# Kernel tuning notes

Hardware: AMD Instinct MI355X
Metric: run time of the kernel (lower is better)

## Reference

```python
import jax, jax.numpy as jnp
import numpy as np

H = 16      # headNum
C = 64      # cDim
D = 1024    # qDim = kDim = vDim = outDim
N = 2       # batch
S = 1024    # seq len


def setup_inputs() -> dict:
    key = jax.random.key(0)
    ks = jax.random.split(key, 12)
    inp = {
        "Qin": jax.random.normal(ks[0], (N, S, D), dtype=jnp.float32),
        "Kin": jax.random.normal(ks[1], (N, S, D), dtype=jnp.float32),
        "Vin": jax.random.normal(ks[2], (N, S, D), dtype=jnp.float32),
        "seqMask": jax.random.randint(ks[3], (N, S), 0, 2).astype(jnp.bool_),
        "attMask": jax.random.normal(ks[4], (1, 1, S, S), dtype=jnp.float32),
        # learned parameters (stored as [in, out] for x @ W)
        "QTrans": jax.random.normal(ks[5], (D, H * C), dtype=jnp.float32) * 0.02,
        "KTrans": jax.random.normal(ks[6], (D, H * C), dtype=jnp.float32) * 0.02,
        "VTrans": jax.random.normal(ks[7], (D, H * C), dtype=jnp.float32) * 0.02,
        "GTrans_w": jax.random.normal(ks[8], (D, H * C), dtype=jnp.float32) * 0.02,
        "GTrans_b": jnp.ones((H * C,), dtype=jnp.float32),
        "out_w": jax.random.normal(ks[9], (H * C, D), dtype=jnp.float32) * 0.02,
        "out_b": jnp.zeros((D,), dtype=jnp.float32),
    }
    return inp


def _split_heads(x):
    # [n, s, h*c] -> [h, n, s, c]
    n, s, _ = x.shape
    return x.reshape(n, s, H, C).transpose(2, 0, 1, 3)


def reference(Qin, Kin, Vin, seqMask, attMask, QTrans, KTrans, VTrans,
              GTrans_w, GTrans_b, out_w, out_b):
    Q = _split_heads(Qin @ QTrans)                         # [h,n,s,c]
    K = _split_heads(Kin @ KTrans)                         # [h,n,t,c]
    V = _split_heads(Vin @ VTrans)                         # [h,n,t,c]
    G = jax.nn.sigmoid(_split_heads(Vin @ GTrans_w + GTrans_b))  # [h,n,s,c]

    scale = 1.0 / jnp.sqrt(jnp.float32(C))
    A = jnp.einsum('hnsi,hnti->hnst', Q, K) * scale        # [h,n,s,t]
    # masked_fill where outer-product of seqMask is True
    m = (seqMask[:, :, None] & seqMask[:, None, :])[None]  # [1,n,s,t]
    A = jnp.where(m, -jnp.inf, A)
    A = A + attMask
    A = jax.nn.softmax(A, axis=-1)
    # gated attention-value reduction (eval mode: dropout inactive)
    O = jnp.einsum('hnst,hnti,hnsi->nshi', A, V, G)        # [n,s,h,c]
    O = O.reshape(O.shape[0], O.shape[1], -1)              # [n,s,h*c]
    return O @ out_w + out_b
```

## Files before the change

kernel.cpp:

```cpp
#include <hip/hip_runtime.h>
#include <hip/hip_bf16.h>
#include <cstddef>

#define S_   1024
#define HC_  1024
#define C_   64
#define LOG2E 1.4426950408889634f
#define SC2   0.18033688011112042f

typedef __attribute__((ext_vector_type(8))) short bf16x8;
typedef __attribute__((ext_vector_type(4))) short bf16x4;
typedef __attribute__((ext_vector_type(4))) float f32x4;

typedef __attribute__((address_space(1))) const void gconst_t;
typedef __attribute__((address_space(3))) void lds_t;

__device__ __forceinline__ short cvt_bf16(float f) {
  union { float f; unsigned u; } v; v.f = f;
  unsigned r = v.u + 0x7FFFu + ((v.u >> 16) & 1u);
  return (short)(r >> 16);
}
__device__ __forceinline__ float bf2f(short s) {
  union { float f; unsigned u; } v; v.u = ((unsigned)(unsigned short)s) << 16;
  return v.f;
}

template<int N> __device__ __forceinline__ void wait_vm() {
  if constexpr (N == 0)       asm volatile("s_waitcnt vmcnt(0)" ::: "memory");
  else if constexpr (N == 2)  asm volatile("s_waitcnt vmcnt(2)" ::: "memory");
  else if constexpr (N == 4)  asm volatile("s_waitcnt vmcnt(4)" ::: "memory");
  else if constexpr (N == 6)  asm volatile("s_waitcnt vmcnt(6)" ::: "memory");
  else if constexpr (N == 8)  asm volatile("s_waitcnt vmcnt(8)" ::: "memory");
  else if constexpr (N == 12) asm volatile("s_waitcnt vmcnt(12)" ::: "memory");
}

__global__ __launch_bounds__(256) void prep(
    const float* __restrict__ QT, const float* __restrict__ KT,
    const float* __restrict__ VT, const float* __restrict__ GW,
    const float* __restrict__ OW, short* __restrict__ WTb,
    const float* __restrict__ Qin, const float* __restrict__ Kin,
    const float* __restrict__ Vin, short* __restrict__ Abf,
    const float* __restrict__ att, const unsigned char* __restrict__ sm,
    short* __restrict__ biasP) {
  __shared__ short tile[32][33];
  __shared__ int a1, a4;
  const int bid = blockIdx.x;
  const int t = threadIdx.x;

  if (bid < 5120) {
    const int which = bid >> 10, xb = bid & 1023;
    const float* src = (which == 0) ? QT : (which == 1) ? KT : (which == 2) ? VT
                      : (which == 3) ? GW : OW;
    short* dst = WTb + (size_t)which * (1024u * 1024u);
    const int tj = (xb & 31) * 32;
    const int tk = (xb >> 5) * 32;
    const int r = t >> 3, c4 = (t & 7) * 4;
    const float4 v = *(const float4*)(src + (size_t)(tk + r) * 1024 + tj + c4);
    tile[c4 + 0][r] = cvt_bf16(v.x);
    tile[c4 + 1][r] = cvt_bf16(v.y);
    tile[c4 + 2][r] = cvt_bf16(v.z);
    tile[c4 + 3][r] = cvt_bf16(v.w);
    __syncthreads();
    bf16x4 o;
    o[0] = tile[r][c4 + 0]; o[1] = tile[r][c4 + 1];
    o[2] = tile[r][c4 + 2]; o[3] = tile[r][c4 + 3];
    *(bf16x4*)(dst + (size_t)(tj + r) * 1024 + tk + c4) = o;
  } else if (bid < 8192) {
    const int idx = bid - 5120;
    const int y = idx >> 10, xb = idx & 1023;
    const float* src = (y == 0) ? Qin : (y == 1) ? Kin : Vin;
    short* d = Abf + (size_t)y * 2097152u;
    const int i = (xb * 256 + t) * 8;
    const float4 a = *(const float4*)(src + i);
    const float4 b = *(const float4*)(src + i + 4);
    bf16x8 o;
    o[0] = cvt_bf16(a.x); o[1] = cvt_bf16(a.y); o[2] = cvt_bf16(a.z); o[3] = cvt_bf16(a.w);
    o[4] = cvt_bf16(b.x); o[5] = cvt_bf16(b.y); o[6] = cvt_bf16(b.z); o[7] = cvt_bf16(b.w);
    *(bf16x8*)(d + i) = o;
  } else {
    if (t == 0) { a1 = 0; a4 = 0; }
    __syncthreads();
    int l1 = 0, l4 = 0;
    for (int i = t; i < 2048; i += 256) {
      if (sm[i]) { if (i & 3) l1 = 1; else if (i & 4) l4 = 1; }
    }
    if (l1) atomicOr(&a1, 1);
    if (l4) atomicOr(&a4, 1);
    __syncthreads();
    const int mst = a1 ? 1 : (a4 ? 4 : 8);

    const int idx = bid - 8192;
    const int qw = idx & 63, tt = (idx >> 6) & 15, n = idx >> 10;
    const int lslot = t >> 2, i4 = t & 3;
    const int tc = tt * 64 + i4 * 16 + (lslot & 15);
    const int qbase = qw * 16 + ((lslot >> 4) << 2);
    const int smt = sm[(size_t)(n * 1024 + tc) * mst];
    bf16x4 o;
#pragma unroll
    for (int ii = 0; ii < 4; ii++) {
      const int q = qbase + ii;
      const int smq = sm[(size_t)(n * 1024 + q) * mst];
      const float val = (smq && smt) ? -1e4f : att[(size_t)q * 1024 + tc] * LOG2E;
      o[ii] = cvt_bf16(val);
    }
    short* dst = biasP + (((size_t)(n * 64 + qw) * 16 + tt) * 64 + lslot) * 16 + i4 * 4;
    *(bf16x4*)dst = o;
  }
}

__global__ __launch_bounds__(256) void v_transpose(
    const short* __restrict__ Vp, short* __restrict__ VpT) {
  __shared__ short tile[32][33];
  const int n = blockIdx.y;
  const int tc = (blockIdx.x & 31) * 32;
  const int ts = (blockIdx.x >> 5) * 32;
  const int t = threadIdx.x;
  const int r = t >> 3, c4 = (t & 7) * 4;
  bf16x4 v = *(const bf16x4*)(Vp + (size_t)(n * S_ + ts + r) * HC_ + tc + c4);
  tile[c4 + 0][r] = v[0]; tile[c4 + 1][r] = v[1];
  tile[c4 + 2][r] = v[2]; tile[c4 + 3][r] = v[3];
  __syncthreads();
  bf16x4 o;
  o[0] = tile[r][c4 + 0]; o[1] = tile[r][c4 + 1];
  o[2] = tile[r][c4 + 2]; o[3] = tile[r][c4 + 3];
  *(bf16x4*)(VpT + ((size_t)n * HC_ + tc + r) * S_ + ts + c4) = o;
}

template<int MW, int NW>
__device__ __forceinline__ void gemm_core_bf(
    const short* __restrict__ A, const short* __restrict__ BT,
    short* As, short* Bs, int m0, int n0, f32x4 acc[MW][NW]) {
  const int t = threadIdx.x;
  const int lane = t & 63, wid = t >> 6;
  const int wr = wid >> 1, wc = wid & 1;
  const int l15 = lane & 15, g = lane >> 4;
  constexpr int NT = 32;
  constexpr int LDT = MW / 2 + NW / 2;
  constexpr int ABUF = MW * 1024;
  constexpr int BBUF = NW * 1024;

#pragma unroll
  for (int m = 0; m < MW; m++)
#pragma unroll
    for (int n2 = 0; n2 < NW; n2++) acc[m][n2] = (f32x4){0.f, 0.f, 0.f, 0.f};

#define STAGE_(buf, kt)                                                        \
  {                                                                            \
    const int k0_ = (kt) * 32;                                                 \
    _Pragma("unroll")                                                          \
    for (int i_ = 0; i_ < NW / 2; i_++) {                                      \
      const int seg_ = i_ * 256 + t;                                           \
      const int row_ = seg_ >> 2, gl_ = seg_ & 3;                              \
      __builtin_amdgcn_global_load_lds(                                        \
          (gconst_t*)(BT + (size_t)(n0 + row_) * 1024 + k0_ +                  \
                      ((gl_ ^ ((row_ >> 1) & 3)) * 8)),                        \
          (lds_t*)(Bs + (buf) * BBUF + seg_ * 8), 16, 0, 0);                   \
    }                                                                          \
    _Pragma("unroll")                                                          \
    for (int i_ = 0; i_ < MW / 2; i_++) {                                      \
      const int seg_ = i_ * 256 + t;                                           \
      const int row_ = seg_ >> 2, gl_ = seg_ & 3;                              \
      __builtin_amdgcn_global_load_lds(                                        \
          (gconst_t*)(A + (size_t)(m0 + row_) * 1024 + k0_ +                   \
                      ((gl_ ^ ((row_ >> 1) & 3)) * 8)),                        \
          (lds_t*)(As + (buf) * ABUF + seg_ * 8), 16, 0, 0);                   \
    }                                                                          \
  }

  STAGE_(0, 0);
  STAGE_(1, 1);
  STAGE_(2, 2);
  int b0 = 0, b1 = 1, b2 = 2, b3 = 3;
  for (int kt = 0; kt < NT; ++kt) {
    if (kt + 3 < NT) {
      STAGE_(b3, kt + 3);
      wait_vm<3 * LDT>();
    } else if (kt + 3 == NT) {
      wait_vm<2 * LDT>();
    } else if (kt + 2 == NT) {
      wait_vm<LDT>();
    } else {
      wait_vm<0>();
    }
    __builtin_amdgcn_sched_barrier(0);
    __builtin_amdgcn_s_barrier();
    __builtin_amdgcn_sched_barrier(0);

    const short* Ac = As + b0 * ABUF;
    const short* Bc = Bs + b0 * BBUF;
    bf16x8 a[MW], b[NW];
#pragma unroll
    for (int m = 0; m < MW; m++) {
      const int row = wr * (MW * 16) + m * 16 + l15;
      a[m] = *(const bf16x8*)(Ac + row * 32 + ((g ^ ((row >> 1) & 3)) * 8));
    }
#pragma unroll
    for (int n2 = 0; n2 < NW; n2++) {
      const int row = wc * (NW * 16) + n2 * 16 + l15;
      b[n2] = *(const bf16x8*)(Bc + row * 32 + ((g ^ ((row >> 1) & 3)) * 8));
    }
    __builtin_amdgcn_s_setprio(1);
#pragma unroll
    for (int m = 0; m < MW; m++)
#pragma unroll
      for (int n2 = 0; n2 < NW; n2++)
        acc[m][n2] = __builtin_amdgcn_mfma_f32_16x16x32_bf16(a[m], b[n2], acc[m][n2], 0, 0, 0);
    __builtin_amdgcn_s_setprio(0);
    __builtin_amdgcn_sched_barrier(0);
    __builtin_amdgcn_s_barrier();
    __builtin_amdgcn_sched_barrier(0);
    const int tmp = b0; b0 = b1; b1 = b2; b2 = b3; b3 = tmp;
  }
#undef STAGE_
}

__global__ __launch_bounds__(256) void gemm_proj(
    const short* __restrict__ Abf, const short* __restrict__ WTb,
    short* __restrict__ Pb, const float* __restrict__ gb) {
  __shared__ short As[4 * 4096];
  __shared__ short Bs[4 * 4096];
  const int bid = blockIdx.x;
  const int xcd = bid & 7, ord = bid >> 3;
  const int y = xcd >> 1, nh = xcd & 1;
  const int m0 = (ord & 15) * 128;
  const int n0 = (nh * 4 + (ord >> 4)) * 128;
  const short* A = Abf + (size_t)((y <= 2) ? y : 2) * 2097152u;
  const short* BT = WTb + (size_t)y * (1024u * 1024u);
  short* outp = Pb + (size_t)y * 2097152u;
  f32x4 acc[4][4];
  gemm_core_bf<4, 4>(A, BT, As, Bs, m0, n0, acc);
  const int t = threadIdx.x, lane = t & 63, wid = t >> 6;
  const int wr = wid >> 1, wc = wid & 1, l15 = lane & 15, g = lane >> 4;
#pragma unroll
  for (int m = 0; m < 4; m++)
#pragma unroll
    for (int n2 = 0; n2 < 4; n2++)
#pragma unroll
      for (int j = 0; j < 4; j++) {
        const int row = m0 + wr * 64 + m * 16 + g * 4 + j;
        const int col = n0 + wc * 64 + n2 * 16 + l15;
        float v = acc[m][n2][j];
        if (y == 3) { v += gb[col]; v = 1.0f / (1.0f + __expf(-v)); }
        outp[(size_t)row * 1024 + col] = cvt_bf16(v);
      }
}

__global__ __launch_bounds__(256) void gemm_final(
    const short* __restrict__ Aobuf, const short* __restrict__ WTo,
    float* __restrict__ outp, const float* __restrict__ ob) {
  __shared__ short As[4 * 2048];
  __shared__ short Bs[4 * 2048];
  const int bid = blockIdx.x;
  const int xcd = bid & 7, ord = bid >> 3;
  const int mg = xcd >> 1, ng = xcd & 1;
  const int m0 = (mg * 8 + (ord & 7)) * 64;
  const int n0 = (ng * 8 + (ord >> 3)) * 64;
  f32x4 acc[2][2];
  gemm_core_bf<2, 2>(Aobuf, WTo, As, Bs, m0, n0, acc);
  const int t = threadIdx.x, lane = t & 63, wid = t >> 6;
  const int wr = wid >> 1, wc = wid & 1, l15 = lane & 15, g = lane >> 4;
#pragma unroll
  for (int m = 0; m < 2; m++)
#pragma unroll
    for (int n2 = 0; n2 < 2; n2++)
#pragma unroll
      for (int j = 0; j < 4; j++) {
        const int row = m0 + wr * 32 + m * 16 + g * 4 + j;
        const int col = n0 + wc * 32 + n2 * 16 + l15;
        outp[(size_t)row * 1024 + col] = acc[m][n2][j] + ob[col];
      }
}

__global__ __launch_bounds__(256) void attn_split(
    const short* __restrict__ Qp, const short* __restrict__ Kp,
    const short* __restrict__ VpT, const short* __restrict__ biasP,
    float* __restrict__ mlbuf, short* __restrict__ OpartB, int lns) {
  __shared__ short Ks[64 * 64];
  __shared__ short Vt[64 * 64];
  __shared__ short Pl[4][16 * 64];

  const int t = threadIdx.x;
  const int lane = t & 63, w = t >> 6;
  const int l15 = lane & 15, g = lane >> 4;
  const int xb = blockIdx.x, h = blockIdx.y, n = blockIdx.z;
  const int sp = xb & ((1 << lns) - 1), qb = xb >> lns;
  const int itc = 16 >> lns;

  const int sbase = qb * 64 + w * 16;
  const short* qptr = Qp + (size_t)(n * S_ + sbase + l15) * HC_ + h * C_;
  const bf16x8 qf0 = *(const bf16x8*)(qptr + g * 8);
  const bf16x8 qf1 = *(const bf16x8*)(qptr + 32 + g * 8);

  float mrow[4], lsum[4];
  f32x4 oacc[4];
#pragma unroll
  for (int j = 0; j < 4; j++) { mrow[j] = -1e30f; lsum[j] = 0.f; }
#pragma unroll
  for (int cb = 0; cb < 4; cb++) oacc[cb] = (f32x4){0.f, 0.f, 0.f, 0.f};

  const int str = t >> 3, sc8 = (t & 7) * 8;
  const short* bbase = biasP + ((size_t)(n * 64 + qb * 4 + w) * 16 * 64 + lane) * 16;

  {
    const int t0 = sp * itc * 64;
    bf16x8 kA0 = *(const bf16x8*)(Kp + (size_t)(n * S_ + t0 + str) * HC_ + h * C_ + sc8);
    bf16x8 kA1 = *(const bf16x8*)(Kp + (size_t)(n * S_ + t0 + 32 + str) * HC_ + h * C_ + sc8);
    bf16x8 vA0 = *(const bf16x8*)(VpT + ((size_t)n * HC_ + h * C_ + str) * S_ + t0 + sc8);
    bf16x8 vA1 = *(const bf16x8*)(VpT + ((size_t)n * HC_ + h * C_ + 32 + str) * S_ + t0 + sc8);

    for (int it = 0; it < itc; ++it) {
      const int tg = sp * itc + it;
      __syncthreads();
      { const int kr = str;      *(bf16x8*)((char*)Ks + kr * 128 + ((sc8 * 2) ^ ((kr & 7) << 4))) = kA0; }
      { const int kr = 32 + str; *(bf16x8*)((char*)Ks + kr * 128 + ((sc8 * 2) ^ ((kr & 7) << 4))) = kA1; }
      { const int cr = str;      *(bf16x8*)((char*)Vt + cr * 128 + ((sc8 * 2) ^ ((cr & 7) << 4))) = vA0; }
      { const int cr = 32 + str; *(bf16x8*)((char*)Vt + cr * 128 + ((sc8 * 2) ^ ((cr & 7) << 4))) = vA1; }
      __syncthreads();

      const bf16x8 bf0 = *(const bf16x8*)(bbase + tg * 1024);
      const bf16x8 bf1 = *(const bf16x8*)(bbase + tg * 1024 + 8);
      const int t1 = ((it + 1 < itc) ? (tg + 1) : tg) * 64;
      bf16x8 kB0 = *(const bf16x8*)(Kp + (size_t)(n * S_ + t1 + str) * HC_ + h * C_ + sc8);
      bf16x8 kB1 = *(const bf16x8*)(Kp + (size_t)(n * S_ + t1 + 32 + str) * HC_ + h * C_ + sc8);
      bf16x8 vB0 = *(const bf16x8*)(VpT + ((size_t)n * HC_ + h * C_ + str) * S_ + t1 + sc8);
      bf16x8 vB1 = *(const bf16x8*)(VpT + ((size_t)n * HC_ + h * C_ + 32 + str) * S_ + t1 + sc8);

      f32x4 sacc[4];
#pragma unroll
      for (int nb = 0; nb < 4; nb++) sacc[nb] = (f32x4){0.f, 0.f, 0.f, 0.f};
      __builtin_amdgcn_s_setprio(1);
#pragma unroll
      for (int nb = 0; nb < 4; nb++) {
        const int krow = nb * 16 + l15;
        const bf16x8 b0 = *(const bf16x8*)((char*)Ks + krow * 128 + ((g * 16) ^ ((krow & 7) << 4)));
        const bf16x8 b1 = *(const bf16x8*)((char*)Ks + krow * 128 + ((64 + g * 16) ^ ((krow & 7) << 4)));
        sacc[nb] = __builtin_amdgcn_mfma_f32_16x16x32_bf16(qf0, b0, sacc[nb], 0, 0, 0);
        sacc[nb] = __builtin_amdgcn_mfma_f32_16x16x32_bf16(qf1, b1, sacc[nb], 0, 0, 0);
      }
      __builtin_amdgcn_s_setprio(0);

      float tmax[4];
#pragma unroll
      for (int j = 0; j < 4; j++) tmax[j] = -1e30f;
#pragma unroll
      for (int nb = 0; nb < 4; nb++)
#pragma unroll
        for (int j = 0; j < 4; j++) {
          const short bb = (nb < 2) ? bf0[nb * 4 + j] : bf1[(nb - 2) * 4 + j];
          const float lg = sacc[nb][j] * SC2 + bf2f(bb);
          sacc[nb][j] = lg;
          tmax[j] = fmaxf(tmax[j], lg);
        }
#pragma unroll
      for (int j = 0; j < 4; j++) {
#pragma unroll
        for (int d = 1; d < 16; d <<= 1)
          tmax[j] = fmaxf(tmax[j], __shfl_xor(tmax[j], d, 64));
        const float mn = fmaxf(mrow[j], tmax[j]);
        const float sc = exp2f(mrow[j] - mn);
        mrow[j] = mn;
        lsum[j] *= sc;
#pragma unroll
        for (int cb = 0; cb < 4; cb++) oacc[cb][j] *= sc;
        float ps = 0.f;
#pragma unroll
        for (int nb = 0; nb < 4; nb++) {
          const float p = exp2f(sacc[nb][j] - mn);
          sacc[nb][j] = p;
          ps += p;
        }
        lsum[j] += ps;
      }
      short* Pw = &Pl[w][0];
#pragma unroll
      for (int nb = 0; nb < 4; nb++)
#pragma unroll
        for (int j = 0; j < 4; j++) {
          const int pr = g * 4 + j;
          const int pcb = (nb * 16 + l15) * 2;
          *(short*)((char*)Pw + pr * 128 + (pcb ^ ((pr & 7) << 4))) = cvt_bf16(sacc[nb][j]);
        }
      __builtin_amdgcn_s_setprio(1);
#pragma unroll
      for (int kk = 0; kk < 2; kk++) {
        const bf16x8 pf = *(const bf16x8*)((char*)Pw + l15 * 128 + ((kk * 64 + g * 16) ^ ((l15 & 7) << 4)));
#pragma unroll
        for (int cb = 0; cb < 4; cb++) {
          const int vrow = cb * 16 + l15;
          const bf16x8 vf = *(const bf16x8*)((char*)Vt + vrow * 128 + ((kk * 64 + g * 16) ^ ((vrow & 7) << 4)));
          oacc[cb] = __builtin_amdgcn_mfma_f32_16x16x32_bf16(pf, vf, oacc[cb], 0, 0, 0);
        }
      }
      __builtin_amdgcn_s_setprio(0);
      kA0 = kB0; kA1 = kB1; vA0 = vB0; vA1 = vB1;
    }
  }
  const int slot = (((n * 16 + h) * 16 + qb) << lns) + sp;
  short* op = OpartB + (size_t)slot * 4096;
  float* mlp = mlbuf + (size_t)slot * 128;
#pragma unroll
  for (int j = 0; j < 4; j++) {
    float rs = lsum[j];
#pragma unroll
    for (int d = 1; d < 16; d <<= 1) rs += __shfl_xor(rs, d, 64);
    const int row = w * 16 + g * 4 + j;
#pragma unroll
    for (int cb = 0; cb < 4; cb++)
      op[row * 64 + cb * 16 + l15] = cvt_bf16(oacc[cb][j]);
    if (l15 == 0) { mlp[row * 2] = mrow[j]; mlp[row * 2 + 1] = rs; }
  }
}

__global__ __launch_bounds__(256) void attn_merge(
    const short* __restrict__ OpartB, const float* __restrict__ mlbuf,
    const short* __restrict__ Gp, short* __restrict__ ObufB, int lns) {
  const int qb = blockIdx.x, h = blockIdx.y, n = blockIdx.z;
  const int nsplit = 1 << lns;
  const int t = threadIdx.x;
  const int r = t >> 2, c0 = (t & 3) * 16;
  const int bslot = ((n * 16 + h) * 16 + qb) << lns;
  const float* mlb = mlbuf + (size_t)bslot * 128 + r * 2;

  float M = -1e30f;
  for (int sp = 0; sp < nsplit; sp++) M = fmaxf(M, mlb[(size_t)sp * 128]);
  float l = 0.f;
  for (int sp = 0; sp < nsplit; sp++)
    l += exp2f(mlb[(size_t)sp * 128] - M) * mlb[(size_t)sp * 128 + 1];
  const float inv = 1.0f / l;

  float acc[16];
#pragma unroll
  for (int k = 0; k < 16; k++) acc[k] = 0.f;
  for (int sp = 0; sp < nsplit; sp++) {
    const float wsc = exp2f(mlb[(size_t)sp * 128] - M);
    const short* op = OpartB + (size_t)(bslot + sp) * 4096 + r * 64 + c0;
    const bf16x8 v0 = *(const bf16x8*)(op);
    const bf16x8 v1 = *(const bf16x8*)(op + 8);
#pragma unroll
    for (int k = 0; k < 8; k++) {
      acc[k]     += wsc * bf2f(v0[k]);
      acc[8 + k] += wsc * bf2f(v1[k]);
    }
  }
  const int srow = qb * 64 + r;
  const size_t idx = (size_t)(n * S_ + srow) * HC_ + h * C_ + c0;
  const bf16x8 g0 = *(const bf16x8*)(Gp + idx);
  const bf16x8 g1 = *(const bf16x8*)(Gp + idx + 8);
  bf16x8 o0, o1;
#pragma unroll
  for (int k = 0; k < 8; k++) {
    o0[k] = cvt_bf16(acc[k] * inv * bf2f(g0[k]));
    o1[k] = cvt_bf16(acc[8 + k] * inv * bf2f(g1[k]));
  }
  *(bf16x8*)(ObufB + idx) = o0;
  *(bf16x8*)(ObufB + idx + 8) = o1;
}

extern "C" void kernel_launch(void* const* d_in, const int* in_sizes, int n_in,
                              void* d_out, int out_size, void* d_ws, size_t ws_size,
                              hipStream_t stream) {
  const float* Qin      = (const float*)d_in[0];
  const float* Kin      = (const float*)d_in[1];
  const float* Vin      = (const float*)d_in[2];
  const void*  seqMask  = d_in[3];
  const float* attMask  = (const float*)d_in[4];
  const float* QTrans   = (const float*)d_in[5];
  const float* KTrans   = (const float*)d_in[6];
  const float* VTrans   = (const float*)d_in[7];
  const float* GTrans_w = (const float*)d_in[8];
  const float* GTrans_b = (const float*)d_in[9];
  const float* out_w    = (const float*)d_in[10];
  const float* out_b    = (const float*)d_in[11];
  float* out = (float*)d_out;

  char* ws = (char*)d_ws;
  const size_t MB = 1048576u;
  short* WTb   = (short*)(ws);
  short* Abf   = (short*)(ws + 10 * MB);
  short* Pb    = (short*)(ws + 22 * MB);
  short* VpT   = (short*)(ws + 38 * MB);
  short* ObufB = (short*)(ws + 42 * MB);
  short* biasP = (short*)(ws + 46 * MB);
  const size_t partBase = 51 * MB;

  const short* Kp = Pb + (size_t)1u * 2097152u;
  const short* Gp = Pb + (size_t)3u * 2097152u;

  int lns = 0;
  for (int c = 2; c >= 0; c--) {
    const size_t slots = 512u << c;
    if (ws_size >= partBase + slots * (8192u + 512u)) { lns = c; break; }
  }
  const size_t slots = 512u << lns;
  short* OpartB = (short*)(ws + partBase);
  float* mlbuf  = (float*)(ws + partBase + slots * 8192u);

  hipLaunchKernelGGL(prep, dim3(10240), dim3(256), 0, stream,
                     QTrans, KTrans, VTrans, GTrans_w, out_w, WTb,
                     Qin, Kin, Vin, Abf,
                     attMask, (const unsigned char*)seqMask, biasP);
  hipLaunchKernelGGL(gemm_proj, dim3(512), dim3(256), 0, stream,
                     Abf, WTb, Pb, GTrans_b);
  hipLaunchKernelGGL(v_transpose, dim3(1024, 2), dim3(256), 0, stream,
                     Pb + (size_t)2u * 2097152u, VpT);
  hipLaunchKernelGGL(attn_split, dim3(16 << lns, 16, 2), dim3(256), 0, stream,
                     Pb, Kp, VpT, biasP, mlbuf, OpartB, lns);
  hipLaunchKernelGGL(attn_merge, dim3(16, 16, 2), dim3(256), 0, stream,
                     OpartB, mlbuf, Gp, ObufB, lns);
  hipLaunchKernelGGL(gemm_final, dim3(512), dim3(256), 0, stream,
                     ObufB, WTb + (size_t)4u * 1048576u, out, out_b);
}
```

Before: 118.2 us.

## Fuse V transpose into projection GEMM epilogue and cap attention split count

The V-projection blocks of gemm_proj now transpose their output tile through LDS and write V directly in the transposed [n, hc, s] layout, so the separate v_transpose kernel and its extra read/write pass over V are removed. The maximum key-split factor for attention drops from 4 to 2, which lowers the partial-output traffic and merge work at the cost of fewer parallel blocks. The transposed store uses 16-byte vector writes from a 128x128 LDS tile that reuses the A staging buffer. That staging write is strided and may cause LDS bank conflicts.

```diff
diff --git a/kernel.cpp b/kernel.cpp
--- a/kernel.cpp
+++ b/kernel.cpp
@@ -108,24 +108,6 @@
   }
 }
 
-__global__ __launch_bounds__(256) void v_transpose(
-    const short* __restrict__ Vp, short* __restrict__ VpT) {
-  __shared__ short tile[32][33];
-  const int n = blockIdx.y;
-  const int tc = (blockIdx.x & 31) * 32;
-  const int ts = (blockIdx.x >> 5) * 32;
-  const int t = threadIdx.x;
-  const int r = t >> 3, c4 = (t & 7) * 4;
-  bf16x4 v = *(const bf16x4*)(Vp + (size_t)(n * S_ + ts + r) * HC_ + tc + c4);
-  tile[c4 + 0][r] = v[0]; tile[c4 + 1][r] = v[1];
-  tile[c4 + 2][r] = v[2]; tile[c4 + 3][r] = v[3];
-  __syncthreads();
-  bf16x4 o;
-  o[0] = tile[r][c4 + 0]; o[1] = tile[r][c4 + 1];
-  o[2] = tile[r][c4 + 2]; o[3] = tile[r][c4 + 3];
-  *(bf16x4*)(VpT + ((size_t)n * HC_ + tc + r) * S_ + ts + c4) = o;
-}
-
 template<int MW, int NW>
 __device__ __forceinline__ void gemm_core_bf(
     const short* __restrict__ A, const short* __restrict__ BT,
@@ -216,7 +198,8 @@
 
 __global__ __launch_bounds__(256) void gemm_proj(
     const short* __restrict__ Abf, const short* __restrict__ WTb,
-    short* __restrict__ Pb, const float* __restrict__ gb) {
+    short* __restrict__ Pb, short* __restrict__ VpT,
+    const float* __restrict__ gb) {
   __shared__ short As[4 * 4096];
   __shared__ short Bs[4 * 4096];
   const int bid = blockIdx.x;
@@ -226,23 +209,48 @@
   const int n0 = (nh * 4 + (ord >> 4)) * 128;
   const short* A = Abf + (size_t)((y <= 2) ? y : 2) * 2097152u;
   const short* BT = WTb + (size_t)y * (1024u * 1024u);
-  short* outp = Pb + (size_t)y * 2097152u;
   f32x4 acc[4][4];
   gemm_core_bf<4, 4>(A, BT, As, Bs, m0, n0, acc);
   const int t = threadIdx.x, lane = t & 63, wid = t >> 6;
   const int wr = wid >> 1, wc = wid & 1, l15 = lane & 15, g = lane >> 4;
-#pragma unroll
-  for (int m = 0; m < 4; m++)
-#pragma unroll
-    for (int n2 = 0; n2 < 4; n2++)
-#pragma unroll
-      for (int j = 0; j < 4; j++) {
-        const int row = m0 + wr * 64 + m * 16 + g * 4 + j;
-        const int col = n0 + wc * 64 + n2 * 16 + l15;
-        float v = acc[m][n2][j];
-        if (y == 3) { v += gb[col]; v = 1.0f / (1.0f + __expf(-v)); }
-        outp[(size_t)row * 1024 + col] = cvt_bf16(v);
-      }
+
+  if (y == 2) {
+    short* Tr = As;
+#pragma unroll
+    for (int m = 0; m < 4; m++)
+#pragma unroll
+      for (int n2 = 0; n2 < 4; n2++)
+#pragma unroll
+        for (int j = 0; j < 4; j++) {
+          const int r = wr * 64 + m * 16 + g * 4 + j;
+          const int c = wc * 64 + n2 * 16 + l15;
+          Tr[c * 128 + r] = cvt_bf16(acc[m][n2][j]);
+        }
+    __syncthreads();
+    const int nz = (m0 >= 1024) ? 1 : 0;
+    const int sbase = m0 & 1023;
+#pragma unroll
+    for (int p = 0; p < 8; p++) {
+      const int unit = p * 256 + t;
+      const int cl = unit >> 4, sr8 = unit & 15;
+      const bf16x8 v = *(const bf16x8*)(Tr + cl * 128 + sr8 * 8);
+      *(bf16x8*)(VpT + ((size_t)(nz * 1024 + n0 + cl)) * 1024 + sbase + sr8 * 8) = v;
+    }
+  } else {
+    short* outp = Pb + (size_t)y * 2097152u;
+#pragma unroll
+    for (int m = 0; m < 4; m++)
+#pragma unroll
+      for (int n2 = 0; n2 < 4; n2++)
+#pragma unroll
+        for (int j = 0; j < 4; j++) {
+          const int row = m0 + wr * 64 + m * 16 + g * 4 + j;
+          const int col = n0 + wc * 64 + n2 * 16 + l15;
+          float v = acc[m][n2][j];
+          if (y == 3) { v += gb[col]; v = 1.0f / (1.0f + __expf(-v)); }
+          outp[(size_t)row * 1024 + col] = cvt_bf16(v);
+        }
+  }
 }
 
 __global__ __launch_bounds__(256) void gemm_final(
@@ -487,7 +495,7 @@
   const short* Gp = Pb + (size_t)3u * 2097152u;
 
   int lns = 0;
-  for (int c = 2; c >= 0; c--) {
+  for (int c = 1; c >= 0; c--) {
     const size_t slots = 512u << c;
     if (ws_size >= partBase + slots * (8192u + 512u)) { lns = c; break; }
   }
@@ -500,9 +508,7 @@
                      Qin, Kin, Vin, Abf,
                      attMask, (const unsigned char*)seqMask, biasP);
   hipLaunchKernelGGL(gemm_proj, dim3(512), dim3(256), 0, stream,
-                     Abf, WTb, Pb, GTrans_b);
-  hipLaunchKernelGGL(v_transpose, dim3(1024, 2), dim3(256), 0, stream,
-                     Pb + (size_t)2u * 2097152u, VpT);
+                     Abf, WTb, Pb, VpT, GTrans_b);
   hipLaunchKernelGGL(attn_split, dim3(16 << lns, 16, 2), dim3(256), 0, stream,
                      Pb, Kp, VpT, biasP, mlbuf, OpartB, lns);
   hipLaunchKernelGGL(attn_merge, dim3(16, 16, 2), dim3(256), 0, stream,
```

Measured after the change: 112.2 us. 5.0% less time.
